# Performance work log

Measured on AMD Instinct MI355X. Metric: run time of the kernel, lower is better.

The kernel has to match this reference:

```python
import jax, jax.numpy as jnp
import numpy as np

EPS = 1e-6


def setup_inputs() -> dict:
    key = jax.random.key(0)
    k1, k2, k3, k4 = jax.random.split(key, 4)
    B, N, D = 8, 4096, 512
    x = jax.random.normal(k1, (B, N, D), dtype=jnp.float32)
    # torch nn.Linear(dim, 3*dim, bias=False): weight shape [3D, D], y = x @ W.T
    w_qkv = jax.random.normal(k2, (3 * D, D), dtype=jnp.float32) * (1.0 / np.sqrt(D))
    w_proj = jax.random.normal(k3, (D, D), dtype=jnp.float32) * (1.0 / np.sqrt(D))
    b_proj = jax.random.normal(k4, (D,), dtype=jnp.float32) * 0.01
    return {"x": x, "w_qkv": w_qkv, "w_proj": w_proj, "b_proj": b_proj, "heads": 8}


def reference(x, w_qkv, w_proj, b_proj, heads):
    B, N, D = x.shape
    H = heads
    d = D // H
    # qkv projection -> (3, B, H, N, d)
    qkv = (x @ w_qkv.T).reshape(B, N, 3, H, d).transpose(2, 0, 3, 1, 4)
    q, k, v = qkv[0], qkv[1], qkv[2]
    # elu+1 feature map (positive features)
    q = jax.nn.elu(q) + 1.0 + EPS
    k = jax.nn.elu(k) + 1.0 + EPS
    # kv summary: [B,H,d,d]
    kv = jnp.einsum('bhnd,bhne->bhde', k, v)
    # denominator: q . sum_n(k) -> [B,H,N]
    denom = jnp.einsum('bhnd,bhd->bhn', q, k.sum(axis=2))
    out = jnp.einsum('bhnd,bhde->bhne', q, kv) / (denom[..., None] + EPS)
    out = out.transpose(0, 2, 1, 3).reshape(B, N, D)
    return out @ w_proj.T + b_proj
```

## Files before the change

kernel.cpp:

```cpp
#include <hip/hip_runtime.h>
#include <hip/hip_bf16.h>
#include <math.h>

#define EPSF 1e-6f

constexpr int Bc = 8;
constexpr int Nc = 4096;
constexpr int Dc = 512;
constexpr int QKVC = 3 * Dc;

typedef __attribute__((ext_vector_type(8))) short short8v;
typedef __attribute__((ext_vector_type(8))) unsigned short ushort8v;
typedef __attribute__((ext_vector_type(4))) float float4v;

__device__ __forceinline__ unsigned short f2bf(float f) {
    union { float f; unsigned int u; } v; v.f = f;
    unsigned int u = v.u;
    return (unsigned short)((u + 0x7fffu + ((u >> 16) & 1u)) >> 16);
}
__device__ __forceinline__ float bf2f(unsigned short h) {
    union { unsigned int u; float f; } v; v.u = ((unsigned int)h) << 16;
    return v.f;
}

typedef __attribute__((address_space(1))) const void gvoid_t;
typedef __attribute__((address_space(3))) void lvoid_t;
__device__ __forceinline__ void llds16(const void* g, void* l) {
    __builtin_amdgcn_global_load_lds((gvoid_t*)g, (lvoid_t*)l, 16, 0, 0);
}

__global__ __launch_bounds__(256) void cvt_f32_bf16(
    const float* __restrict__ in, unsigned short* __restrict__ out, int n8)
{
    int i = blockIdx.x * 256 + threadIdx.x;
    if (i >= n8) return;
    float4 a = reinterpret_cast<const float4*>(in)[2 * i];
    float4 b = reinterpret_cast<const float4*>(in)[2 * i + 1];
    ushort8v o;
    o[0] = f2bf(a.x); o[1] = f2bf(a.y); o[2] = f2bf(a.z); o[3] = f2bf(a.w);
    o[4] = f2bf(b.x); o[5] = f2bf(b.y); o[6] = f2bf(b.z); o[7] = f2bf(b.w);
    reinterpret_cast<ushort8v*>(out)[i] = o;
}

template <int ELU_COLS, bool BIAS, bool OUT_BF16>
__global__ __launch_bounds__(256) void gemm_bf16(
    const unsigned short* __restrict__ A, int lda,
    const unsigned short* __restrict__ Bm, int ldb,
    void* __restrict__ Cout, int ldc, int K,
    const float* __restrict__ bias)
{
    __shared__ unsigned short lA[2][128 * 32];
    __shared__ unsigned short lB[2][128 * 32];

    const int t    = threadIdx.x;
    const int bm   = blockIdx.x * 128;
    const int bn   = blockIdx.y * 128;
    const int w    = t >> 6, lane = t & 63;
    const int ln   = lane & 15, g = lane >> 4;
    const int wr   = (w >> 1) * 64, wc = (w & 1) * 64;

    const int r0  = t >> 2;
    const int ks0 = (t & 3) * 8;
    const unsigned short* Ap0 = A + (size_t)(bm + r0) * lda + ks0;
    const unsigned short* Ap1 = A + (size_t)(bm + r0 + 64) * lda + ks0;
    const unsigned short* Bp0 = Bm + (size_t)(bn + r0) * ldb + ks0;
    const unsigned short* Bp1 = Bm + (size_t)(bn + r0 + 64) * ldb + ks0;

    float4v acc[4][4];
#pragma unroll
    for (int i = 0; i < 4; ++i)
#pragma unroll
        for (int j = 0; j < 4; ++j) acc[i][j] = {0.f, 0.f, 0.f, 0.f};

    const int nt = K >> 5;

#define STAGE_T(buf, k0) do { \
        llds16(Ap0 + (k0), lA[buf] + (size_t)t * 8); \
        llds16(Ap1 + (k0), lA[buf] + (size_t)(t + 256) * 8); \
        llds16(Bp0 + (k0), lB[buf] + (size_t)t * 8); \
        llds16(Bp1 + (k0), lB[buf] + (size_t)(t + 256) * 8); \
    } while (0)

    STAGE_T(0, 0);
    __syncthreads();

    int cur = 0;
    for (int tt = 0; tt < nt; ++tt) {
        if (tt + 1 < nt) STAGE_T(cur ^ 1, (tt + 1) << 5);

        const unsigned short* pa = lA[cur];
        const unsigned short* pb = lB[cur];
        short8v a[4], b[4];
#pragma unroll
        for (int i = 0; i < 4; ++i)
            a[i] = *reinterpret_cast<const short8v*>(pa + (wr + i * 16 + ln) * 32 + g * 8);
#pragma unroll
        for (int j = 0; j < 4; ++j)
            b[j] = *reinterpret_cast<const short8v*>(pb + (wc + j * 16 + ln) * 32 + g * 8);

        __builtin_amdgcn_s_setprio(1);
#pragma unroll
        for (int i = 0; i < 4; ++i)
#pragma unroll
            for (int j = 0; j < 4; ++j)
                acc[i][j] = __builtin_amdgcn_mfma_f32_16x16x32_bf16(a[i], b[j], acc[i][j], 0, 0, 0);
        __builtin_amdgcn_s_setprio(0);

        __syncthreads();
        cur ^= 1;
    }
#undef STAGE_T

#pragma unroll
    for (int i = 0; i < 4; ++i) {
        const int Rb = bm + wr + i * 16 + g * 4;
#pragma unroll
        for (int j = 0; j < 4; ++j) {
            const int Cc = bn + wc + j * 16 + ln;
            const bool do_elu = (ELU_COLS > 0) && (Cc < ELU_COLS);
            float bv = BIAS ? bias[Cc] : 0.f;
#pragma unroll
            for (int r = 0; r < 4; ++r) {
                float v = acc[i][j][r];
                if (do_elu) v = (v > 0.f) ? (v + 1.0f + EPSF) : (expf(v) + EPSF);
                if (BIAS) v += bv;
                if (OUT_BF16)
                    ((unsigned short*)Cout)[(size_t)(Rb + r) * ldc + Cc] = f2bf(v);
                else
                    ((float*)Cout)[(size_t)(Rb + r) * ldc + Cc] = v;
            }
        }
    }
}

__global__ __launch_bounds__(256) void kv_part(
    const unsigned short* __restrict__ qkv,
    float* __restrict__ kvp, float* __restrict__ ksp)
{
    const int bh = blockIdx.x, chunk = blockIdx.y;
    const int b = bh >> 3, h = bh & 7;

    __shared__ float kt[64][68];
    __shared__ float vt[64][68];
    __shared__ float ksl[4][64];

    const int t  = threadIdx.x;
    const int e  = t & 63, dg = t >> 6;
    const int rr = t >> 3, slot = t & 7;

    float acc[16] = {};
    float ks = 0.f;

    const size_t base = ((size_t)b * Nc + (size_t)chunk * 512) * QKVC + h * 64;

    for (int n0 = 0; n0 < 512; n0 += 64) {
#pragma unroll
        for (int half = 0; half < 2; ++half) {
            const int row = rr + half * 32;
            const unsigned short* kr = qkv + base + (size_t)(n0 + row) * QKVC + Dc + slot * 8;
            const unsigned short* vr = kr + Dc;
            ushort8v kq = *reinterpret_cast<const ushort8v*>(kr);
            ushort8v vq = *reinterpret_cast<const ushort8v*>(vr);
            float4 k0 = make_float4(bf2f(kq[0]), bf2f(kq[1]), bf2f(kq[2]), bf2f(kq[3]));
            float4 k1 = make_float4(bf2f(kq[4]), bf2f(kq[5]), bf2f(kq[6]), bf2f(kq[7]));
            float4 v0 = make_float4(bf2f(vq[0]), bf2f(vq[1]), bf2f(vq[2]), bf2f(vq[3]));
            float4 v1 = make_float4(bf2f(vq[4]), bf2f(vq[5]), bf2f(vq[6]), bf2f(vq[7]));
            *reinterpret_cast<float4*>(&kt[row][slot * 8])     = k0;
            *reinterpret_cast<float4*>(&kt[row][slot * 8 + 4]) = k1;
            *reinterpret_cast<float4*>(&vt[row][slot * 8])     = v0;
            *reinterpret_cast<float4*>(&vt[row][slot * 8 + 4]) = v1;
        }
        __syncthreads();
#pragma unroll 2
        for (int nn = 0; nn < 64; ++nn) {
            const float vv = vt[nn][e];
            const float4 q0 = *reinterpret_cast<const float4*>(&kt[nn][dg * 16]);
            const float4 q1 = *reinterpret_cast<const float4*>(&kt[nn][dg * 16 + 4]);
            const float4 q2 = *reinterpret_cast<const float4*>(&kt[nn][dg * 16 + 8]);
            const float4 q3 = *reinterpret_cast<const float4*>(&kt[nn][dg * 16 + 12]);
            acc[0]  += q0.x * vv; acc[1]  += q0.y * vv; acc[2]  += q0.z * vv; acc[3]  += q0.w * vv;
            acc[4]  += q1.x * vv; acc[5]  += q1.y * vv; acc[6]  += q1.z * vv; acc[7]  += q1.w * vv;
            acc[8]  += q2.x * vv; acc[9]  += q2.y * vv; acc[10] += q2.z * vv; acc[11] += q2.w * vv;
            acc[12] += q3.x * vv; acc[13] += q3.y * vv; acc[14] += q3.z * vv; acc[15] += q3.w * vv;
        }
#pragma unroll
        for (int nn = 0; nn < 16; ++nn) ks += kt[dg * 16 + nn][e];
        __syncthreads();
    }

    float* kvpp = kvp + ((size_t)bh * 8 + chunk) * 4096;
#pragma unroll
    for (int i = 0; i < 16; ++i) kvpp[(dg * 16 + i) * 64 + e] = acc[i];

    ksl[dg][e] = ks;
    __syncthreads();
    if (t < 64) ksp[((size_t)bh * 8 + chunk) * 64 + t] =
        ksl[0][t] + ksl[1][t] + ksl[2][t] + ksl[3][t];
}

__global__ __launch_bounds__(256) void kv_reduce(
    const float* __restrict__ kvp, const float* __restrict__ ksp,
    unsigned short* __restrict__ kvT, float* __restrict__ ksum)
{
    const int bh = blockIdx.x, t = threadIdx.x;
    const float* src = kvp + (size_t)bh * 8 * 4096;
#pragma unroll
    for (int i = 0; i < 16; ++i) {
        const int idx = i * 256 + t;
        float s = 0.f;
#pragma unroll
        for (int c = 0; c < 8; ++c) s += src[c * 4096 + idx];
        const int d = idx >> 6, e = idx & 63;
        kvT[(size_t)bh * 4096 + e * 64 + d] = f2bf(s);
    }
    if (t < 64) {
        float s = 0.f;
#pragma unroll
        for (int c = 0; c < 8; ++c) s += ksp[((size_t)bh * 8 + c) * 64 + t];
        ksum[bh * 64 + t] = s;
    }
}

__global__ __launch_bounds__(256) void attn_proj(
    const unsigned short* __restrict__ qkv,
    const unsigned short* __restrict__ kvT,
    const float* __restrict__ ksum,
    const unsigned short* __restrict__ wp,
    const float* __restrict__ bias,
    float* __restrict__ out)
{
    __shared__ unsigned short lq[128 * 64];
    __shared__ unsigned short lkv[64 * 64];
    __shared__ unsigned short lwp[128 * 64];
    __shared__ unsigned short loL[128 * 64];

    const int t = threadIdx.x;
    const int rowBlk = blockIdx.x;
    const int bn = blockIdx.y;
    const int b = rowBlk >> 5;
    const size_t rowBase = (size_t)rowBlk * 128;

    const int w = t >> 6, lane = t & 63;
    const int ln = lane & 15, g = lane >> 4;
    const int wr = (w >> 1) * 64, wc = (w & 1) * 64;
    const int l7 = ln & 7;

    char* lqc  = (char*)lq;
    char* lkvc = (char*)lkv;
    char* lwpc = (char*)lwp;
    char* loLc = (char*)loL;

    float4v accP[4][4];
#pragma unroll
    for (int i = 0; i < 4; ++i)
#pragma unroll
        for (int j = 0; j < 4; ++j) accP[i][j] = {0.f, 0.f, 0.f, 0.f};

    for (int h = 0; h < 8; ++h) {
        const int bh = b * 8 + h;
        const unsigned short* qsrc = qkv + rowBase * QKVC + h * 64;
        const unsigned short* wsrc = wp + (size_t)(bn * 128) * 512 + h * 64;
        const unsigned short* ksrc = kvT + (size_t)bh * 4096;

#pragma unroll
        for (int s = 0; s < 4; ++s) {
            const int c = s * 256 + t, r = c >> 3, ci = c & 7;
            ushort8v qv = *reinterpret_cast<const ushort8v*>(qsrc + (size_t)r * QKVC + ci * 8);
            *reinterpret_cast<ushort8v*>(lqc + r * 128 + ((ci ^ (r & 7)) << 4)) = qv;
            ushort8v wv = *reinterpret_cast<const ushort8v*>(wsrc + (size_t)r * 512 + ci * 8);
            *reinterpret_cast<ushort8v*>(lwpc + r * 128 + ((ci ^ (r & 7)) << 4)) = wv;
        }
#pragma unroll
        for (int s = 0; s < 2; ++s) {
            const int c = s * 256 + t, r = c >> 3, ci = c & 7;
            ushort8v kvv = *reinterpret_cast<const ushort8v*>(ksrc + r * 64 + ci * 8);
            *reinterpret_cast<ushort8v*>(lkvc + r * 128 + ((ci ^ (r & 7)) << 4)) = kvv;
        }
        __syncthreads();

        float ksv[2][8];
        {
            const float* ksb = ksum + bh * 64 + g * 8;
            float4 a0 = *reinterpret_cast<const float4*>(ksb);
            float4 a1 = *reinterpret_cast<const float4*>(ksb + 4);
            float4 b0 = *reinterpret_cast<const float4*>(ksb + 32);
            float4 b1 = *reinterpret_cast<const float4*>(ksb + 36);
            ksv[0][0] = a0.x; ksv[0][1] = a0.y; ksv[0][2] = a0.z; ksv[0][3] = a0.w;
            ksv[0][4] = a1.x; ksv[0][5] = a1.y; ksv[0][6] = a1.z; ksv[0][7] = a1.w;
            ksv[1][0] = b0.x; ksv[1][1] = b0.y; ksv[1][2] = b0.z; ksv[1][3] = b0.w;
            ksv[1][4] = b1.x; ksv[1][5] = b1.y; ksv[1][6] = b1.z; ksv[1][7] = b1.w;
        }

        short8v akv[4][2], bq[2][2];
#pragma unroll
        for (int i = 0; i < 4; ++i)
#pragma unroll
            for (int kk = 0; kk < 2; ++kk)
                akv[i][kk] = *reinterpret_cast<const short8v*>(
                    lkvc + (i * 16 + ln) * 128 + (((kk * 4 + g) ^ l7) << 4));
#pragma unroll
        for (int j = 0; j < 2; ++j)
#pragma unroll
            for (int kk = 0; kk < 2; ++kk)
                bq[j][kk] = *reinterpret_cast<const short8v*>(
                    lqc + (w * 32 + j * 16 + ln) * 128 + (((kk * 4 + g) ^ l7) << 4));

        float4v acco[4][2];
#pragma unroll
        for (int i = 0; i < 4; ++i)
#pragma unroll
            for (int j = 0; j < 2; ++j) acco[i][j] = {0.f, 0.f, 0.f, 0.f};
#pragma unroll
        for (int kk = 0; kk < 2; ++kk)
#pragma unroll
            for (int i = 0; i < 4; ++i)
#pragma unroll
                for (int j = 0; j < 2; ++j)
                    acco[i][j] = __builtin_amdgcn_mfma_f32_16x16x32_bf16(
                        akv[i][kk], bq[j][kk], acco[i][j], 0, 0, 0);

        float inv[2];
#pragma unroll
        for (int j = 0; j < 2; ++j) {
            float p = 0.f;
#pragma unroll
            for (int kk = 0; kk < 2; ++kk)
#pragma unroll
                for (int m = 0; m < 8; ++m)
                    p += bf2f((unsigned short)bq[j][kk][m]) * ksv[kk][m];
            p += __shfl_xor(p, 16);
            p += __shfl_xor(p, 32);
            inv[j] = 1.0f / (p + EPSF);
        }

#pragma unroll
        for (int i = 0; i < 4; ++i)
#pragma unroll
            for (int j = 0; j < 2; ++j) {
                unsigned int p0 = (unsigned int)f2bf(acco[i][j][0] * inv[j]) |
                                  ((unsigned int)f2bf(acco[i][j][1] * inv[j]) << 16);
                unsigned int p1 = (unsigned int)f2bf(acco[i][j][2] * inv[j]) |
                                  ((unsigned int)f2bf(acco[i][j][3] * inv[j]) << 16);
                const int row = w * 32 + j * 16 + ln;
                const int chunk = i * 2 + (g >> 1);
                char* dst = loLc + row * 128 + (((chunk ^ l7) << 4) | ((g & 1) << 3));
                *reinterpret_cast<uint2*>(dst) = make_uint2(p0, p1);
            }
        __syncthreads();

        short8v ao[4][2], bw[4][2];
#pragma unroll
        for (int i = 0; i < 4; ++i)
#pragma unroll
            for (int kk = 0; kk < 2; ++kk)
                ao[i][kk] = *reinterpret_cast<const short8v*>(
                    loLc + (wr + i * 16 + ln) * 128 + (((kk * 4 + g) ^ l7) << 4));
#pragma unroll
        for (int j = 0; j < 4; ++j)
#pragma unroll
            for (int kk = 0; kk < 2; ++kk)
                bw[j][kk] = *reinterpret_cast<const short8v*>(
                    lwpc + (wc + j * 16 + ln) * 128 + (((kk * 4 + g) ^ l7) << 4));

        __builtin_amdgcn_s_setprio(1);
#pragma unroll
        for (int kk = 0; kk < 2; ++kk)
#pragma unroll
            for (int i = 0; i < 4; ++i)
#pragma unroll
                for (int j = 0; j < 4; ++j)
                    accP[i][j] = __builtin_amdgcn_mfma_f32_16x16x32_bf16(
                        ao[i][kk], bw[j][kk], accP[i][j], 0, 0, 0);
        __builtin_amdgcn_s_setprio(0);
        __syncthreads();
    }

#pragma unroll
    for (int j = 0; j < 4; ++j) {
        const int col = bn * 128 + wc + j * 16 + ln;
        const float bv = bias[col];
#pragma unroll
        for (int i = 0; i < 4; ++i) {
            const size_t rg = rowBase + wr + i * 16 + g * 4;
#pragma unroll
            for (int rr = 0; rr < 4; ++rr)
                out[(rg + rr) * 512 + col] = accP[i][j][rr] + bv;
        }
    }
}

extern "C" void kernel_launch(void* const* d_in, const int* in_sizes, int n_in,
                              void* d_out, int out_size, void* d_ws, size_t ws_size,
                              hipStream_t stream)
{
    const float* x      = (const float*)d_in[0];
    const float* w_qkv  = (const float*)d_in[1];
    const float* w_proj = (const float*)d_in[2];
    const float* b_proj = (const float*)d_in[3];
    float* out = (float*)d_out;

    char* ws = (char*)d_ws;
    unsigned short* qkvb = (unsigned short*)ws;
    size_t off = (size_t)32768 * 1536 * 2;
    unsigned short* xb   = (unsigned short*)(ws + off); off += (size_t)32768 * 512 * 2;
    unsigned short* wqb  = (unsigned short*)(ws + off); off += (size_t)1536 * 512 * 2;
    unsigned short* wpb  = (unsigned short*)(ws + off); off += (size_t)512 * 512 * 2;
    float* kvp           = (float*)(ws + off);          off += (size_t)64 * 8 * 4096 * 4;
    float* ksp           = (float*)(ws + off);          off += (size_t)64 * 8 * 64 * 4;
    unsigned short* kvT  = (unsigned short*)(ws + off); off += (size_t)64 * 4096 * 2;
    float* ksumb         = (float*)(ws + off);

    cvt_f32_bf16<<<dim3((32768 * 512 / 8 + 255) / 256), dim3(256), 0, stream>>>(x, xb, 32768 * 512 / 8);
    cvt_f32_bf16<<<dim3((1536 * 512 / 8 + 255) / 256), dim3(256), 0, stream>>>(w_qkv, wqb, 1536 * 512 / 8);
    cvt_f32_bf16<<<dim3((512 * 512 / 8 + 255) / 256), dim3(256), 0, stream>>>(w_proj, wpb, 512 * 512 / 8);

    gemm_bf16<1024, false, true><<<dim3(256, 12), dim3(256), 0, stream>>>(
        xb, Dc, wqb, Dc, qkvb, QKVC, Dc, nullptr);

    kv_part<<<dim3(64, 8), dim3(256), 0, stream>>>(qkvb, kvp, ksp);
    kv_reduce<<<dim3(64), dim3(256), 0, stream>>>(kvp, ksp, kvT, ksumb);

    attn_proj<<<dim3(256, 4), dim3(256), 0, stream>>>(
        qkvb, kvT, ksumb, wpb, b_proj, out);
}
```

Measured before the change: 203.8 us.

## Rewrite QKV GEMM with 256x128 tiles, 3-stage LDS ring, swizzle, XCD remap

Replaces the generic bf16 GEMM for the QKV projection with a specialized kernel. It uses 512-thread blocks on 256x128 tiles with a K-step of 64 and a triple-buffered LDS ring. Loads are tracked with explicit vmcnt waits and raw barriers instead of __syncthreads. An XOR swizzle on LDS rows aims to cut bank conflicts, and a block-index remap spreads tiles across XCDs for better L2 reuse. The goal is more latency hiding and fewer LDS stalls in the largest GEMM, at the cost of 144KB of LDS per block, which limits occupancy and adds fragile hand-tuned waitcnt logic.

Result: faster. 195.2 us (-4.2%).

```diff
diff --git a/kernel.cpp b/kernel.cpp
--- a/kernel.cpp
+++ b/kernel.cpp
@@ -42,29 +42,48 @@
     reinterpret_cast<ushort8v*>(out)[i] = o;
 }
 
-template <int ELU_COLS, bool BIAS, bool OUT_BF16>
-__global__ __launch_bounds__(256) void gemm_bf16(
-    const unsigned short* __restrict__ A, int lda,
-    const unsigned short* __restrict__ Bm, int ldb,
-    void* __restrict__ Cout, int ldc, int K,
-    const float* __restrict__ bias)
-{
-    __shared__ unsigned short lA[2][128 * 32];
-    __shared__ unsigned short lB[2][128 * 32];
-
-    const int t    = threadIdx.x;
-    const int bm   = blockIdx.x * 128;
-    const int bn   = blockIdx.y * 128;
-    const int w    = t >> 6, lane = t & 63;
-    const int ln   = lane & 15, g = lane >> 4;
-    const int wr   = (w >> 1) * 64, wc = (w & 1) * 64;
-
-    const int r0  = t >> 2;
-    const int ks0 = (t & 3) * 8;
-    const unsigned short* Ap0 = A + (size_t)(bm + r0) * lda + ks0;
-    const unsigned short* Ap1 = A + (size_t)(bm + r0 + 64) * lda + ks0;
-    const unsigned short* Bp0 = Bm + (size_t)(bn + r0) * ldb + ks0;
-    const unsigned short* Bp1 = Bm + (size_t)(bn + r0 + 64) * ldb + ks0;
+__global__ __launch_bounds__(512, 2) void gemm_qkv(
+    const unsigned short* __restrict__ A,
+    const unsigned short* __restrict__ Bm,
+    unsigned short* __restrict__ Cout)
+{
+    constexpr int LDA = 512, LDB = 512, LDC = 1536;
+    constexpr int NT = 8;
+    __shared__ unsigned short ring[3][24576];
+
+    const int t = threadIdx.x;
+    const int orig = blockIdx.x;
+    const int wg = (orig & 7) * 192 + (orig >> 3);
+    const int bm = (wg / 12) * 256;
+    const int bn = (wg % 12) * 128;
+
+    const int w = t >> 6, lane = t & 63;
+    const int ln = lane & 15, g = lane >> 4;
+    const int wr = (w >> 1) * 64;
+    const int wc = (w & 1) * 64;
+    const int l7 = ln & 7;
+
+    const int rs = t >> 3;
+    const int ci = t & 7;
+    const int swz = ci ^ (rs & 7);
+    const unsigned short* As0 = A + (size_t)(bm + rs) * LDA + swz * 8;
+    const unsigned short* As1 = A + (size_t)(bm + 64 + rs) * LDA + swz * 8;
+    const unsigned short* As2 = A + (size_t)(bm + 128 + rs) * LDA + swz * 8;
+    const unsigned short* As3 = A + (size_t)(bm + 192 + rs) * LDA + swz * 8;
+    const unsigned short* Bs0 = Bm + (size_t)(bn + rs) * LDB + swz * 8;
+    const unsigned short* Bs1 = Bm + (size_t)(bn + 64 + rs) * LDB + swz * 8;
+
+#define STAGEQ(Tt) do {                                                        \
+        const int k0_ = (Tt) * 64;                                             \
+        unsigned short* dA_ = &ring[(Tt) % 3][0];                              \
+        unsigned short* dB_ = &ring[(Tt) % 3][16384];                          \
+        llds16(As0 + k0_, dA_ + (size_t)t * 8);                                \
+        llds16(As1 + k0_, dA_ + (size_t)(512 + t) * 8);                        \
+        llds16(As2 + k0_, dA_ + (size_t)(1024 + t) * 8);                       \
+        llds16(As3 + k0_, dA_ + (size_t)(1536 + t) * 8);                       \
+        llds16(Bs0 + k0_, dB_ + (size_t)t * 8);                                \
+        llds16(Bs1 + k0_, dB_ + (size_t)(512 + t) * 8);                        \
+    } while (0)
 
     float4v acc[4][4];
 #pragma unroll
@@ -72,44 +91,56 @@
 #pragma unroll
         for (int j = 0; j < 4; ++j) acc[i][j] = {0.f, 0.f, 0.f, 0.f};
 
-    const int nt = K >> 5;
-
-#define STAGE_T(buf, k0) do { \
-        llds16(Ap0 + (k0), lA[buf] + (size_t)t * 8); \
-        llds16(Ap1 + (k0), lA[buf] + (size_t)(t + 256) * 8); \
-        llds16(Bp0 + (k0), lB[buf] + (size_t)t * 8); \
-        llds16(Bp1 + (k0), lB[buf] + (size_t)(t + 256) * 8); \
-    } while (0)
-
-    STAGE_T(0, 0);
-    __syncthreads();
-
-    int cur = 0;
-    for (int tt = 0; tt < nt; ++tt) {
-        if (tt + 1 < nt) STAGE_T(cur ^ 1, (tt + 1) << 5);
-
-        const unsigned short* pa = lA[cur];
-        const unsigned short* pb = lB[cur];
-        short8v a[4], b[4];
+    STAGEQ(0);
+    STAGEQ(1);
+    asm volatile("s_waitcnt vmcnt(6)" ::: "memory");
+    __builtin_amdgcn_s_barrier();
+    __builtin_amdgcn_sched_barrier(0);
+
+#pragma unroll
+    for (int T = 0; T < NT; ++T) {
+        if (T + 2 < NT) STAGEQ(T + 2);
+
+        const unsigned short* base = &ring[T % 3][0];
+        short8v a[4][2], b[4][2];
 #pragma unroll
         for (int i = 0; i < 4; ++i)
-            a[i] = *reinterpret_cast<const short8v*>(pa + (wr + i * 16 + ln) * 32 + g * 8);
+#pragma unroll
+            for (int kk = 0; kk < 2; ++kk) {
+                const int row = wr + i * 16 + ln;
+                a[i][kk] = *reinterpret_cast<const short8v*>(
+                    base + row * 64 + (((kk * 4 + g) ^ l7) << 3));
+            }
 #pragma unroll
         for (int j = 0; j < 4; ++j)
-            b[j] = *reinterpret_cast<const short8v*>(pb + (wc + j * 16 + ln) * 32 + g * 8);
+#pragma unroll
+            for (int kk = 0; kk < 2; ++kk) {
+                const int row = wc + j * 16 + ln;
+                b[j][kk] = *reinterpret_cast<const short8v*>(
+                    base + 16384 + row * 64 + (((kk * 4 + g) ^ l7) << 3));
+            }
 
         __builtin_amdgcn_s_setprio(1);
 #pragma unroll
-        for (int i = 0; i < 4; ++i)
-#pragma unroll
-            for (int j = 0; j < 4; ++j)
-                acc[i][j] = __builtin_amdgcn_mfma_f32_16x16x32_bf16(a[i], b[j], acc[i][j], 0, 0, 0);
+        for (int kk = 0; kk < 2; ++kk)
+#pragma unroll
+            for (int i = 0; i < 4; ++i)
+#pragma unroll
+                for (int j = 0; j < 4; ++j)
+                    acc[i][j] = __builtin_amdgcn_mfma_f32_16x16x32_bf16(
+                        a[i][kk], b[j][kk], acc[i][j], 0, 0, 0);
         __builtin_amdgcn_s_setprio(0);
 
-        __syncthreads();
-        cur ^= 1;
-    }
-#undef STAGE_T
+        if (T + 1 < NT) {
+            if (T + 2 < NT)
+                asm volatile("s_waitcnt vmcnt(6)" ::: "memory");
+            else
+                asm volatile("s_waitcnt vmcnt(0)" ::: "memory");
+            __builtin_amdgcn_s_barrier();
+            __builtin_amdgcn_sched_barrier(0);
+        }
+    }
+#undef STAGEQ
 
 #pragma unroll
     for (int i = 0; i < 4; ++i) {
@@ -117,17 +148,12 @@
 #pragma unroll
         for (int j = 0; j < 4; ++j) {
             const int Cc = bn + wc + j * 16 + ln;
-            const bool do_elu = (ELU_COLS > 0) && (Cc < ELU_COLS);
-            float bv = BIAS ? bias[Cc] : 0.f;
+            const bool do_elu = (Cc < 1024);
 #pragma unroll
             for (int r = 0; r < 4; ++r) {
                 float v = acc[i][j][r];
                 if (do_elu) v = (v > 0.f) ? (v + 1.0f + EPSF) : (expf(v) + EPSF);
-                if (BIAS) v += bv;
-                if (OUT_BF16)
-                    ((unsigned short*)Cout)[(size_t)(Rb + r) * ldc + Cc] = f2bf(v);
-                else
-                    ((float*)Cout)[(size_t)(Rb + r) * ldc + Cc] = v;
+                Cout[(size_t)(Rb + r) * LDC + Cc] = f2bf(v);
             }
         }
     }
@@ -414,8 +440,7 @@
     cvt_f32_bf16<<<dim3((1536 * 512 / 8 + 255) / 256), dim3(256), 0, stream>>>(w_qkv, wqb, 1536 * 512 / 8);
     cvt_f32_bf16<<<dim3((512 * 512 / 8 + 255) / 256), dim3(256), 0, stream>>>(w_proj, wpb, 512 * 512 / 8);
 
-    gemm_bf16<1024, false, true><<<dim3(256, 12), dim3(256), 0, stream>>>(
-        xb, Dc, wqb, Dc, qkvb, QKVC, Dc, nullptr);
+    gemm_qkv<<<dim3(1536), dim3(512), 0, stream>>>(xb, wqb, qkvb);
 
     kv_part<<<dim3(64, 8), dim3(256), 0, stream>>>(qkvb, kvp, ksp);
     kv_reduce<<<dim3(64), dim3(256), 0, stream>>>(kvp, ksp, kvT, ksumb);
```
